# Performance work log

Hardware: AMD Instinct MI355X
Metric: run time of the kernel (lower is better)

## Reference

```python
import jax, jax.numpy as jnp
import numpy as np

EPSILON = 0.001
CAP = 2000.0
H, W, C, B = 224, 224, 1024, 256


def setup_inputs() -> dict:
    key = jax.random.key(0)
    k1, k2, k3, k4 = jax.random.split(key, 4)
    x = jax.random.normal(k1, (B, H, W), dtype=jnp.float32)
    positions = 0.5 + 0.3 * jax.random.normal(k2, (1, 1, C, 2), dtype=jnp.float32)
    sigmas = 0.02 * jax.random.normal(k3, (1, 1, C), dtype=jnp.float32)
    curve_weights = 0.2 * jax.random.normal(k4, (1, 1, C), dtype=jnp.float32)
    y_axis = jnp.linspace(0.0, 1.0, H + 1)[:-1]
    x_axis = jnp.linspace(0.0, 1.0, W + 1)[:-1]
    ys, xs = jnp.meshgrid(y_axis, x_axis, indexing='ij')
    return {"x": x, "positions": positions, "sigmas": sigmas,
            "curve_weights": curve_weights, "xs": xs.astype(jnp.float32),
            "ys": ys.astype(jnp.float32)}


def calc_curves(positions, sigmas, curve_weights, xs, ys):
    # sigmas/curve_weights: (1,1,C); xs/ys: (H,W)
    two_sig2 = 2.0 * sigmas ** 2 + EPSILON            # (1,1,C)
    factor = 1.0 / (2.0 * jnp.pi * sigmas ** 2 + EPSILON)
    grid = (xs[:, :, None] - positions[..., 1]) ** 2 + \
           (ys[:, :, None] - positions[..., 0]) ** 2   # (H,W,C)
    curves = factor * jnp.exp(-grid / two_sig2) * curve_weights
    return jnp.clip(curves, -CAP, CAP)                 # (H,W,C)


def reference(x, positions, sigmas, curve_weights, xs, ys):
    x = x.reshape(-1, H, W)
    curves = calc_curves(positions, sigmas, curve_weights, xs, ys)
    num_pixels = float(H * W)
    # sum over H,W of curves[None] * x[...,None]  ==  GEMM contraction
    out = jnp.einsum('bhw,hwc->bc', x, curves) / num_pixels
    return out
```

## Files before the change

kernel.cpp:

```cpp
#include <hip/hip_runtime.h>
#include <hip/hip_bf16.h>
#include <stdint.h>

#define HH 224
#define WW 224
#define CC 1024
#define BB 256
#define KK (HH*WW)
#define EPSILON_F 0.001f
#define LOG2E 1.4426950408889634f
#define INVN (1.0f/50176.0f)
#define CLAMP_V (2000.0f/50176.0f)

#define KCHUNKS 32
#define ROWS_PER_CHUNK 7
#define STEPS 49

#define LDS_STRIDE 36

typedef __bf16 bf16x8 __attribute__((ext_vector_type(8)));
typedef float  f32x4  __attribute__((ext_vector_type(4)));

__global__ __launch_bounds__(256)
void cvt_bf16_kernel(const float* __restrict__ x, __hip_bfloat16* __restrict__ xb, int n8) {
    int i = blockIdx.x * 256 + threadIdx.x;
    if (i >= n8) return;
    const float4* p = (const float4*)(x + (size_t)i * 8);
    float4 a = p[0], b = p[1];
    union { __hip_bfloat16 h[8]; uint4 u; } o;
    o.h[0] = (__hip_bfloat16)a.x; o.h[1] = (__hip_bfloat16)a.y;
    o.h[2] = (__hip_bfloat16)a.z; o.h[3] = (__hip_bfloat16)a.w;
    o.h[4] = (__hip_bfloat16)b.x; o.h[5] = (__hip_bfloat16)b.y;
    o.h[6] = (__hip_bfloat16)b.z; o.h[7] = (__hip_bfloat16)b.w;
    *(uint4*)(xb + (size_t)i * 8) = o.u;
}

__global__ __launch_bounds__(256)
void reduce_kernel(const float* __restrict__ part, float* __restrict__ out) {
    int i = blockIdx.x * 256 + threadIdx.x;
    const f32x4* p = (const f32x4*)part + i;
    f32x4 s = {0.f, 0.f, 0.f, 0.f};
#pragma unroll
    for (int z = 0; z < KCHUNKS; ++z)
        s += p[(size_t)z * (BB * CC / 4)];
    ((f32x4*)out)[i] = s;
}

template <bool BF16A, bool PARTIAL>
__global__ __launch_bounds__(256)
void blob_gemm_kernel(const void* __restrict__ xin,
                      const float* __restrict__ pos,
                      const float* __restrict__ sig,
                      const float* __restrict__ cwt,
                      const float* __restrict__ xs,
                      const float* __restrict__ ys,
                      float* __restrict__ dst) {
    __shared__ __bf16 As[2][256 * LDS_STRIDE];
    __shared__ __bf16 Bs[2][64 * LDS_STRIDE];
    __shared__ float  xrow[WW];
    __shared__ float  ycol[ROWS_PER_CHUNK];

    const int tid  = threadIdx.x;
    const int wave = tid >> 6;
    const int lane = tid & 63;

    const int n  = blockIdx.x;
    const int j  = n >> 3;
    const int z  = (n & 7) * 4 + (j >> 4);
    const int c0 = (j & 15) * 64;
    const int k0 = z * (ROWS_PER_CHUNK * WW);

    if (tid < WW) xrow[tid] = xs[tid];
    if (tid >= WW && tid < WW + ROWS_PER_CHUNK)
        ycol[tid - WW] = ys[(z * ROWS_PER_CHUNK + (tid - WW)) * WW];

    const int q   = tid & 3;
    const int cr0 = tid >> 2;
    const int c   = c0 + cr0;
    float A2, S2, P0, P1;
    {
        float s  = sig[c];
        float w  = cwt[c];
        float s2 = s * s;
        A2 = w / (6.283185307179586f * s2 + EPSILON_F) * INVN;
        S2 = LOG2E / (2.0f * s2 + EPSILON_F);
        P0 = pos[2 * c];
        P1 = pos[2 * c + 1];
    }

    const __hip_bfloat16* agb[4];
    const float* agf[4];
#pragma unroll
    for (int jj = 0; jj < 4; ++jj) {
        size_t off = (size_t)(cr0 + 64 * jj) * KK + k0 + q * 8;
        agb[jj] = (const __hip_bfloat16*)xin + off;
        agf[jj] = (const float*)xin + off;
    }
    const int as_w = cr0 * LDS_STRIDE + q * 8;
    const int bs_w = cr0 * LDS_STRIDE + q * 8;

    const int wm = wave * 64;
    const int fl = lane & 15;
    const int fk = (lane >> 4) * 8;
    const int ar_off = (wm + fl) * LDS_STRIDE + fk;
    const int br_off = fl * LDS_STRIDE + fk;

    f32x4 acc[4][4];
#pragma unroll
    for (int i = 0; i < 4; ++i)
#pragma unroll
        for (int jj = 0; jj < 4; ++jj) acc[i][jj] = (f32x4){0.f, 0.f, 0.f, 0.f};

    __syncthreads();

    float ycolr[ROWS_PER_CHUNK];
#pragma unroll
    for (int r = 0; r < ROWS_PER_CHUNK; ++r) ycolr[r] = ycol[r];

    float Ex[8];
    {
        float4 xv0 = *(const float4*)(xrow + q * 8);
        float4 xv1 = *(const float4*)(xrow + q * 8 + 4);
        float xv[8] = {xv0.x, xv0.y, xv0.z, xv0.w, xv1.x, xv1.y, xv1.z, xv1.w};
#pragma unroll
        for (int i = 0; i < 8; ++i) {
            float dx = xv[i] - P1;
            Ex[i] = __builtin_amdgcn_exp2f(-(dx * S2 * dx));
        }
        float dy  = ycolr[0] - P0;
        float eyA = __builtin_amdgcn_exp2f(-(dy * S2 * dy)) * A2;
        union { __bf16 h[8]; uint4 u; } cv;
#pragma unroll
        for (int i = 0; i < 8; ++i) {
            float v = Ex[i] * eyA;
            cv.h[i] = (__bf16)fminf(fmaxf(v, -CLAMP_V), CLAMP_V);
        }
        *(uint4*)(&Bs[0][bs_w]) = cv.u;
#pragma unroll
        for (int jj = 0; jj < 4; ++jj) {
            union { __bf16 h[8]; uint4 u; } av;
            if (BF16A) {
                av.u = *(const uint4*)(agb[jj]);
            } else {
                float4 f0 = *(const float4*)(agf[jj]);
                float4 f1 = *(const float4*)(agf[jj] + 4);
                av.h[0] = (__bf16)f0.x; av.h[1] = (__bf16)f0.y;
                av.h[2] = (__bf16)f0.z; av.h[3] = (__bf16)f0.w;
                av.h[4] = (__bf16)f1.x; av.h[5] = (__bf16)f1.y;
                av.h[6] = (__bf16)f1.z; av.h[7] = (__bf16)f1.w;
            }
            *(uint4*)(&As[0][as_w + 64 * jj * LDS_STRIDE]) = av.u;
        }
    }
    __syncthreads();

    int nr = 1, nwb = 0;
#pragma unroll 2
    for (int s = 0; s < STEPS; ++s) {
        const int cb = s & 1;

        uint4  pa[4];
        float4 pf0[4], pf1[4];
        if (s < STEPS - 1) {
            const int koff = nr * WW + nwb * 32;
            if (BF16A) {
#pragma unroll
                for (int jj = 0; jj < 4; ++jj) pa[jj] = *(const uint4*)(agb[jj] + koff);
            } else {
#pragma unroll
                for (int jj = 0; jj < 4; ++jj) {
                    pf0[jj] = *(const float4*)(agf[jj] + koff);
                    pf1[jj] = *(const float4*)(agf[jj] + koff + 4);
                }
            }
        }

        bf16x8 fa[4], fb[4];
#pragma unroll
        for (int i = 0; i < 4; ++i) {
            fa[i] = *(const bf16x8*)(&As[cb][ar_off + i * 16 * LDS_STRIDE]);
            fb[i] = *(const bf16x8*)(&Bs[cb][br_off + i * 16 * LDS_STRIDE]);
        }
#pragma unroll
        for (int mi = 0; mi < 4; ++mi)
#pragma unroll
            for (int ni = 0; ni < 4; ++ni)
                acc[mi][ni] = __builtin_amdgcn_mfma_f32_16x16x32_bf16(
                    fa[mi], fb[ni], acc[mi][ni], 0, 0, 0);

        if (s < STEPS - 1) {
            if (nr == 0) {
                float4 xv0 = *(const float4*)(xrow + nwb * 32 + q * 8);
                float4 xv1 = *(const float4*)(xrow + nwb * 32 + q * 8 + 4);
                float xv[8] = {xv0.x, xv0.y, xv0.z, xv0.w, xv1.x, xv1.y, xv1.z, xv1.w};
#pragma unroll
                for (int i = 0; i < 8; ++i) {
                    float dx = xv[i] - P1;
                    Ex[i] = __builtin_amdgcn_exp2f(-(dx * S2 * dx));
                }
            }
            float dy  = ycolr[nr] - P0;
            float eyA = __builtin_amdgcn_exp2f(-(dy * S2 * dy)) * A2;
            union { __bf16 h[8]; uint4 u; } cv;
#pragma unroll
            for (int i = 0; i < 8; ++i) {
                float v = Ex[i] * eyA;
                cv.h[i] = (__bf16)fminf(fmaxf(v, -CLAMP_V), CLAMP_V);
            }
            *(uint4*)(&Bs[cb ^ 1][bs_w]) = cv.u;
#pragma unroll
            for (int jj = 0; jj < 4; ++jj) {
                union { __bf16 h[8]; uint4 u; } av;
                if (BF16A) {
                    av.u = pa[jj];
                } else {
                    av.h[0] = (__bf16)pf0[jj].x; av.h[1] = (__bf16)pf0[jj].y;
                    av.h[2] = (__bf16)pf0[jj].z; av.h[3] = (__bf16)pf0[jj].w;
                    av.h[4] = (__bf16)pf1[jj].x; av.h[5] = (__bf16)pf1[jj].y;
                    av.h[6] = (__bf16)pf1[jj].z; av.h[7] = (__bf16)pf1[jj].w;
                }
                *(uint4*)(&As[cb ^ 1][as_w + 64 * jj * LDS_STRIDE]) = av.u;
            }
            ++nr;
            if (nr == ROWS_PER_CHUNK) { nr = 0; ++nwb; }
        }
        __syncthreads();
    }

    const int orow = (lane >> 4) * 4;
    float* base = PARTIAL ? (dst + (size_t)z * BB * CC) : dst;
#pragma unroll
    for (int mi = 0; mi < 4; ++mi) {
        int m = wm + mi * 16 + orow;
#pragma unroll
        for (int ni = 0; ni < 4; ++ni) {
            int cc = c0 + ni * 16 + fl;
#pragma unroll
            for (int v = 0; v < 4; ++v) {
                if (PARTIAL)
                    base[(size_t)(m + v) * CC + cc] = acc[mi][ni][v];
                else
                    atomicAdd(base + (size_t)(m + v) * CC + cc, acc[mi][ni][v]);
            }
        }
    }
}

extern "C" void kernel_launch(void* const* d_in, const int* in_sizes, int n_in,
                              void* d_out, int out_size, void* d_ws, size_t ws_size,
                              hipStream_t stream) {
    const float* x   = (const float*)d_in[0];
    const float* pos = (const float*)d_in[1];
    const float* sg  = (const float*)d_in[2];
    const float* cw  = (const float*)d_in[3];
    const float* xs  = (const float*)d_in[4];
    const float* ys  = (const float*)d_in[5];
    float* out = (float*)d_out;

    dim3 grid(16 * KCHUNKS);
    const size_t nx   = (size_t)BB * KK;
    const size_t XB   = nx * sizeof(__hip_bfloat16);
    const size_t PART = (size_t)KCHUNKS * BB * CC * 4;
    const int n8 = (int)(nx / 8);

    if (ws_size >= XB + PART) {
        __hip_bfloat16* xb = (__hip_bfloat16*)d_ws;
        float* part = (float*)((char*)d_ws + XB);
        cvt_bf16_kernel<<<(n8 + 255) / 256, 256, 0, stream>>>(x, xb, n8);
        blob_gemm_kernel<true, true><<<grid, 256, 0, stream>>>(xb, pos, sg, cw, xs, ys, part);
        reduce_kernel<<<BB * CC / 4 / 256, 256, 0, stream>>>(part, out);
    } else if (ws_size >= PART) {
        float* part = (float*)d_ws;
        blob_gemm_kernel<false, true><<<grid, 256, 0, stream>>>(x, pos, sg, cw, xs, ys, part);
        reduce_kernel<<<BB * CC / 4 / 256, 256, 0, stream>>>(part, out);
    } else if (ws_size >= XB) {
        __hip_bfloat16* xb = (__hip_bfloat16*)d_ws;
        hipMemsetAsync(out, 0, (size_t)BB * CC * sizeof(float), stream);
        cvt_bf16_kernel<<<(n8 + 255) / 256, 256, 0, stream>>>(x, xb, n8);
        blob_gemm_kernel<true, false><<<grid, 256, 0, stream>>>(xb, pos, sg, cw, xs, ys, out);
    } else {
        hipMemsetAsync(out, 0, (size_t)BB * CC * sizeof(float), stream);
        blob_gemm_kernel<false, false><<<grid, 256, 0, stream>>>(x, pos, sg, cw, xs, ys, out);
    }
}
```

Before: 147.8 us.

## Restructure GEMM main loop with byte arena, XOR buffer flips, and precomputed row exps

The kernel's shared-memory tiles now live in a single byte arena, and the double buffer is switched by XORing address offsets instead of indexing arrays. The 49-step loop becomes a 7x7 nested loop with constant row offsets, which removes the dynamic row and column counters. The y-direction Gaussian factors are computed once up front, and the clamp is skipped per wave when no amplitude can exceed the cap. Generating and storing the B tile is moved ahead of the MFMA block so it can overlap with the matrix ops, at the cost of more registers and a larger LDS arena.

Result: slower. 246.4 us (+66.7%).

```diff
diff --git a/kernel.cpp b/kernel.cpp
--- a/kernel.cpp
+++ b/kernel.cpp
@@ -17,6 +17,10 @@
 #define STEPS 49
 
 #define LDS_STRIDE 36
+#define ROWB (LDS_STRIDE*2)
+#define AS_BYTES (256*ROWB)
+#define BS_OFF   AS_BYTES
+#define HALF     32768
 
 typedef __bf16 bf16x8 __attribute__((ext_vector_type(8)));
 typedef float  f32x4  __attribute__((ext_vector_type(4)));
@@ -55,8 +59,7 @@
                       const float* __restrict__ xs,
                       const float* __restrict__ ys,
                       float* __restrict__ dst) {
-    __shared__ __bf16 As[2][256 * LDS_STRIDE];
-    __shared__ __bf16 Bs[2][64 * LDS_STRIDE];
+    __shared__ __align__(128) unsigned char arena[2 * HALF];
     __shared__ float  xrow[WW];
     __shared__ float  ycol[ROWS_PER_CHUNK];
 
@@ -87,6 +90,7 @@
         P0 = pos[2 * c];
         P1 = pos[2 * c + 1];
     }
+    const bool doClamp = __any(fabsf(A2) > CLAMP_V) != 0;
 
     const __hip_bfloat16* agb[4];
     const float* agf[4];
@@ -96,14 +100,15 @@
         agb[jj] = (const __hip_bfloat16*)xin + off;
         agf[jj] = (const float*)xin + off;
     }
-    const int as_w = cr0 * LDS_STRIDE + q * 8;
-    const int bs_w = cr0 * LDS_STRIDE + q * 8;
+
+    unsigned aw_cur = (unsigned)(cr0 * ROWB + q * 16);
+    unsigned bw_cur = (unsigned)(BS_OFF + cr0 * ROWB + q * 16);
 
     const int wm = wave * 64;
     const int fl = lane & 15;
     const int fk = (lane >> 4) * 8;
-    const int ar_off = (wm + fl) * LDS_STRIDE + fk;
-    const int br_off = fl * LDS_STRIDE + fk;
+    unsigned ar_cur = (unsigned)((wm + fl) * ROWB + fk * 2);
+    unsigned br_cur = (unsigned)(BS_OFF + fl * ROWB + fk * 2);
 
     f32x4 acc[4][4];
 #pragma unroll
@@ -113,9 +118,12 @@
 
     __syncthreads();
 
-    float ycolr[ROWS_PER_CHUNK];
-#pragma unroll
-    for (int r = 0; r < ROWS_PER_CHUNK; ++r) ycolr[r] = ycol[r];
+    float eyA[ROWS_PER_CHUNK];
+#pragma unroll
+    for (int r = 0; r < ROWS_PER_CHUNK; ++r) {
+        float dy = ycol[r] - P0;
+        eyA[r] = __builtin_amdgcn_exp2f(-(dy * S2 * dy)) * A2;
+    }
 
     float Ex[8];
     {
@@ -127,15 +135,17 @@
             float dx = xv[i] - P1;
             Ex[i] = __builtin_amdgcn_exp2f(-(dx * S2 * dx));
         }
-        float dy  = ycolr[0] - P0;
-        float eyA = __builtin_amdgcn_exp2f(-(dy * S2 * dy)) * A2;
+        float v[8];
+#pragma unroll
+        for (int i = 0; i < 8; ++i) v[i] = Ex[i] * eyA[0];
+        if (doClamp) {
+#pragma unroll
+            for (int i = 0; i < 8; ++i) v[i] = fminf(fmaxf(v[i], -CLAMP_V), CLAMP_V);
+        }
         union { __bf16 h[8]; uint4 u; } cv;
 #pragma unroll
-        for (int i = 0; i < 8; ++i) {
-            float v = Ex[i] * eyA;
-            cv.h[i] = (__bf16)fminf(fmaxf(v, -CLAMP_V), CLAMP_V);
-        }
-        *(uint4*)(&Bs[0][bs_w]) = cv.u;
+        for (int i = 0; i < 8; ++i) cv.h[i] = (__bf16)v[i];
+        *(uint4*)(arena + bw_cur) = cv.u;
 #pragma unroll
         for (int jj = 0; jj < 4; ++jj) {
             union { __bf16 h[8]; uint4 u; } av;
@@ -149,82 +159,100 @@
                 av.h[4] = (__bf16)f1.x; av.h[5] = (__bf16)f1.y;
                 av.h[6] = (__bf16)f1.z; av.h[7] = (__bf16)f1.w;
             }
-            *(uint4*)(&As[0][as_w + 64 * jj * LDS_STRIDE]) = av.u;
-        }
-    }
+            *(uint4*)(arena + aw_cur + jj * (64 * ROWB)) = av.u;
+        }
+    }
+    aw_cur ^= HALF; bw_cur ^= HALF;
     __syncthreads();
 
-    int nr = 1, nwb = 0;
-#pragma unroll 2
-    for (int s = 0; s < STEPS; ++s) {
-        const int cb = s & 1;
-
-        uint4  pa[4];
-        float4 pf0[4], pf1[4];
-        if (s < STEPS - 1) {
-            const int koff = nr * WW + nwb * 32;
-            if (BF16A) {
-#pragma unroll
-                for (int jj = 0; jj < 4; ++jj) pa[jj] = *(const uint4*)(agb[jj] + koff);
-            } else {
+#pragma unroll 1
+    for (int g = 0; g < 7; ++g) {
+        const bool lastG = (g == 6);
+        const __hip_bfloat16* agk[4];
+        const float* agkf[4];
+#pragma unroll
+        for (int jj = 0; jj < 4; ++jj) {
+            agk[jj]  = agb[jj] + g * 32;
+            agkf[jj] = agf[jj] + g * 32;
+        }
+#pragma unroll
+        for (int u = 0; u < 7; ++u) {
+            const bool isLast = (u == 6) && lastG;
+            const int koff = (u < 6) ? (u + 1) * WW : 32;
+
+            uint4  pa[4];
+            float4 pf0[4], pf1[4];
+            if (!isLast) {
+                if (BF16A) {
+#pragma unroll
+                    for (int jj = 0; jj < 4; ++jj) pa[jj] = *(const uint4*)(agk[jj] + koff);
+                } else {
+#pragma unroll
+                    for (int jj = 0; jj < 4; ++jj) {
+                        pf0[jj] = *(const float4*)(agkf[jj] + koff);
+                        pf1[jj] = *(const float4*)(agkf[jj] + koff + 4);
+                    }
+                }
+            }
+
+            bf16x8 fa[4], fb[4];
+#pragma unroll
+            for (int i = 0; i < 4; ++i) {
+                fa[i] = *(const bf16x8*)(arena + ar_cur + i * (16 * ROWB));
+                fb[i] = *(const bf16x8*)(arena + br_cur + i * (16 * ROWB));
+            }
+
+            if (!isLast) {
+                if (u == 6) {
+                    float4 xv0 = *(const float4*)(xrow + (g + 1) * 32 + q * 8);
+                    float4 xv1 = *(const float4*)(xrow + (g + 1) * 32 + q * 8 + 4);
+                    float xv[8] = {xv0.x, xv0.y, xv0.z, xv0.w, xv1.x, xv1.y, xv1.z, xv1.w};
+#pragma unroll
+                    for (int i = 0; i < 8; ++i) {
+                        float dx = xv[i] - P1;
+                        Ex[i] = __builtin_amdgcn_exp2f(-(dx * S2 * dx));
+                    }
+                }
+                const float eyAt = (u < 6) ? eyA[u + 1] : eyA[0];
+                float v[8];
+#pragma unroll
+                for (int i = 0; i < 8; ++i) v[i] = Ex[i] * eyAt;
+                if (doClamp) {
+#pragma unroll
+                    for (int i = 0; i < 8; ++i) v[i] = fminf(fmaxf(v[i], -CLAMP_V), CLAMP_V);
+                }
+                union { __bf16 h[8]; uint4 u4; } cv;
+#pragma unroll
+                for (int i = 0; i < 8; ++i) cv.h[i] = (__bf16)v[i];
+                *(uint4*)(arena + bw_cur) = cv.u4;
+            }
+
+#pragma unroll
+            for (int mi = 0; mi < 4; ++mi)
+#pragma unroll
+                for (int ni = 0; ni < 4; ++ni)
+                    acc[mi][ni] = __builtin_amdgcn_mfma_f32_16x16x32_bf16(
+                        fa[mi], fb[ni], acc[mi][ni], 0, 0, 0);
+
+            if (!isLast) {
 #pragma unroll
                 for (int jj = 0; jj < 4; ++jj) {
-                    pf0[jj] = *(const float4*)(agf[jj] + koff);
-                    pf1[jj] = *(const float4*)(agf[jj] + koff + 4);
+                    union { __bf16 h[8]; uint4 u4; } av;
+                    if (BF16A) {
+                        av.u4 = pa[jj];
+                    } else {
+                        av.h[0] = (__bf16)pf0[jj].x; av.h[1] = (__bf16)pf0[jj].y;
+                        av.h[2] = (__bf16)pf0[jj].z; av.h[3] = (__bf16)pf0[jj].w;
+                        av.h[4] = (__bf16)pf1[jj].x; av.h[5] = (__bf16)pf1[jj].y;
+                        av.h[6] = (__bf16)pf1[jj].z; av.h[7] = (__bf16)pf1[jj].w;
+                    }
+                    *(uint4*)(arena + aw_cur + jj * (64 * ROWB)) = av.u4;
                 }
             }
-        }
-
-        bf16x8 fa[4], fb[4];
-#pragma unroll
-        for (int i = 0; i < 4; ++i) {
-            fa[i] = *(const bf16x8*)(&As[cb][ar_off + i * 16 * LDS_STRIDE]);
-            fb[i] = *(const bf16x8*)(&Bs[cb][br_off + i * 16 * LDS_STRIDE]);
-        }
-#pragma unroll
-        for (int mi = 0; mi < 4; ++mi)
-#pragma unroll
-            for (int ni = 0; ni < 4; ++ni)
-                acc[mi][ni] = __builtin_amdgcn_mfma_f32_16x16x32_bf16(
-                    fa[mi], fb[ni], acc[mi][ni], 0, 0, 0);
-
-        if (s < STEPS - 1) {
-            if (nr == 0) {
-                float4 xv0 = *(const float4*)(xrow + nwb * 32 + q * 8);
-                float4 xv1 = *(const float4*)(xrow + nwb * 32 + q * 8 + 4);
-                float xv[8] = {xv0.x, xv0.y, xv0.z, xv0.w, xv1.x, xv1.y, xv1.z, xv1.w};
-#pragma unroll
-                for (int i = 0; i < 8; ++i) {
-                    float dx = xv[i] - P1;
-                    Ex[i] = __builtin_amdgcn_exp2f(-(dx * S2 * dx));
-                }
-            }
-            float dy  = ycolr[nr] - P0;
-            float eyA = __builtin_amdgcn_exp2f(-(dy * S2 * dy)) * A2;
-            union { __bf16 h[8]; uint4 u; } cv;
-#pragma unroll
-            for (int i = 0; i < 8; ++i) {
-                float v = Ex[i] * eyA;
-                cv.h[i] = (__bf16)fminf(fmaxf(v, -CLAMP_V), CLAMP_V);
-            }
-            *(uint4*)(&Bs[cb ^ 1][bs_w]) = cv.u;
-#pragma unroll
-            for (int jj = 0; jj < 4; ++jj) {
-                union { __bf16 h[8]; uint4 u; } av;
-                if (BF16A) {
-                    av.u = pa[jj];
-                } else {
-                    av.h[0] = (__bf16)pf0[jj].x; av.h[1] = (__bf16)pf0[jj].y;
-                    av.h[2] = (__bf16)pf0[jj].z; av.h[3] = (__bf16)pf0[jj].w;
-                    av.h[4] = (__bf16)pf1[jj].x; av.h[5] = (__bf16)pf1[jj].y;
-                    av.h[6] = (__bf16)pf1[jj].z; av.h[7] = (__bf16)pf1[jj].w;
-                }
-                *(uint4*)(&As[cb ^ 1][as_w + 64 * jj * LDS_STRIDE]) = av.u;
-            }
-            ++nr;
-            if (nr == ROWS_PER_CHUNK) { nr = 0; ++nwb; }
-        }
-        __syncthreads();
+
+            __syncthreads();
+            ar_cur ^= HALF; br_cur ^= HALF; aw_cur ^= HALF; bw_cur ^= HALF;
+        }
     }
 
     const int orow = (lane >> 4) * 4;
```
